# Kernel tuning notes

Measured on AMD Instinct MI355X. Metric: run time of the kernel, lower is better.

Reference implementation:

```python
import jax, jax.numpy as jnp
import numpy as np

T, C, H, W, CI = 4, 64, 96, 96, 16
PS, WS, STR0 = 7, 21, 4
KS, KA = 100, 100
SCALE = 10.0


def conv1x1(x, w, b):
    # x: [T,C,H,W], w: [O,C]
    return jnp.einsum('tchw,oc->tohw', x, w) + b[None, :, None, None]


def unfold_clip(x, ps):
    # clipped-boundary unfold: [T,C,H,W] -> [T, H*W, C*ps*ps]
    t, c, h, w = x.shape
    d = jnp.arange(ps)
    ii = jnp.clip(jnp.arange(h)[:, None] + d[None, :], 0, h - 1)  # [H,ps]
    jj = jnp.clip(jnp.arange(w)[:, None] + d[None, :], 0, w - 1)  # [W,ps]
    p = x[:, :, ii]            # [T,C,H,ps,W]
    p = p[:, :, :, :, jj]      # [T,C,H,ps,W,ps]
    p = jnp.transpose(p, (0, 2, 4, 1, 3, 5))  # [T,H,W,C,ps,ps]
    return p.reshape(t, h * w, c * ps * ps)


def setup_inputs() -> dict:
    key = jax.random.key(0)
    ks = jax.random.split(key, 9)
    s = lambda fan: 1.0 / np.sqrt(fan)
    return {
        'vid': jax.random.normal(ks[0], (T, C, H, W), jnp.float32),
        'g_w': jax.random.normal(ks[1], (CI, C), jnp.float32) * s(C),
        'g_b': jax.random.normal(ks[2], (CI,), jnp.float32) * 0.01,
        'theta_w': jax.random.normal(ks[3], (CI, C), jnp.float32) * s(C),
        'theta_b': jax.random.normal(ks[4], (CI,), jnp.float32) * 0.01,
        'phi_w': jax.random.normal(ks[5], (CI, C), jnp.float32) * s(C),
        'phi_b': jax.random.normal(ks[6], (CI,), jnp.float32) * 0.01,
        'W_w': jax.random.normal(ks[7], (C, CI), jnp.float32) * s(CI),
        'W_b': jax.random.normal(ks[8], (C,), jnp.float32) * 0.01,
    }


def reference(vid, g_w, g_b, theta_w, theta_b, phi_w, phi_b, W_w, W_b):
    t, c, h, w = vid.shape
    b1 = conv1x1(vid, g_w, g_b)          # query features  (g)
    b2 = conv1x1(vid, theta_w, theta_b)  # value features  (theta)
    b3 = conv1x1(vid, phi_w, phi_b)      # key features    (phi)

    b1u = unfold_clip(b1, PS)  # [T,HW,D]
    b2u = unfold_clip(b2, PS)
    b3u = unfold_clip(b3, PS)

    # query grid (stride0)
    qi, qj = jnp.meshgrid(jnp.arange(0, h, STR0), jnp.arange(0, w, STR0), indexing='ij')
    qi, qj = qi.reshape(-1), qj.reshape(-1)
    nq = qi.shape[0]
    qflat = qi * w + qj
    b1q = b1u[:, qflat]  # [T,nq,D]

    # centered spatial search window (stride1=1), clipped bounds
    off = jnp.arange(WS) - WS // 2
    ci = jnp.clip(qi[:, None] + off[None, :], 0, h - 1)  # [nq,WS]
    cj = jnp.clip(qj[:, None] + off[None, :], 0, w - 1)
    cand = (ci[:, :, None] * w + cj[:, None, :]).reshape(nq, WS * WS)

    # patch inner-product dists, one window offset at a time (memory-lean)
    def score(cidx):  # cidx: [nq]
        return jnp.einsum('tqd,tqd->tq', b1q, b3u[:, cidx])
    dists = jax.lax.map(score, cand.T)           # [WS*WS,T,nq]
    dists = jnp.transpose(dists, (1, 2, 0))      # [T,nq,WS*WS]

    vals, idx = jax.lax.top_k(dists, KS)
    vals, idx = vals[..., :KA], idx[..., :KA]
    yi = jax.nn.softmax(vals * SCALE, axis=-1)   # [T,nq,KA]

    pos = jnp.take_along_axis(jnp.broadcast_to(cand[None], (t,) + cand.shape), idx, axis=-1)
    patches = b2u[jnp.arange(t)[:, None, None], pos]   # [T,nq,KA,D]
    zi = jnp.einsum('tqk,tqkd->tqd', yi, patches)      # [T,nq,D]

    # fold: overlap-add scatter + counts normalization
    zi = zi.reshape(t, nq, CI, PS, PS).transpose(0, 2, 1, 3, 4).reshape(t, CI, nq * PS * PS)
    d = jnp.arange(PS)
    pi = jnp.clip(qi[:, None] + d[None, :], 0, h - 1)
    pj = jnp.clip(qj[:, None] + d[None, :], 0, w - 1)
    pix = (pi[:, :, None] * w + pj[:, None, :]).reshape(-1)
    acc = jnp.zeros((t, CI, h * w), vid.dtype).at[:, :, pix].add(zi)
    Z = jnp.zeros((h * w,), vid.dtype).at[pix].add(1.0)
    y = (acc / Z).reshape(t, CI, h, w)

    return vid + conv1x1(y, W_w, W_b)
```

## Files before the change

### kernel.cpp

```cpp
#include <hip/hip_runtime.h>
#include <hip/hip_bf16.h>
#include <hip/hip_fp16.h>
#include <math.h>

typedef __hip_bfloat16 bf16;
typedef unsigned int u32;
typedef unsigned long long u64;
typedef __attribute__((ext_vector_type(8))) short short8;
typedef __attribute__((ext_vector_type(4))) float float4v;

#define T_   4
#define C_   64
#define H_   96
#define W_   96
#define CI_  16
#define HW_  9216
#define NC_  441
#define K_   100
#define HSEL 0x07060302u
#define LSEL 0x05040100u

__device__ __forceinline__ float ldbf(const void* p, int i) { return __bfloat162float(((const bf16*)p)[i]); }
__device__ __forceinline__ float ldf (const void* p, int i) { return ((const float*)p)[i]; }

__device__ __forceinline__ unsigned short f2bf(float x) {
    union { float f; u32 u; } a; a.f = x;
    u32 r = a.u + 0x7FFF + ((a.u >> 16) & 1);
    return (unsigned short)(r >> 16);
}
__device__ __forceinline__ float bf2f(unsigned short s) {
    union { u32 u; float f; } a; a.u = ((u32)s) << 16;
    return a.f;
}
__device__ __forceinline__ u32 packbf(float x) {
    unsigned short h = f2bf(x);
    unsigned short l = f2bf(x - bf2f(h));
    return ((u32)h << 16) | (u32)l;
}
__device__ __forceinline__ u32 okey(float f) {
    u32 u = __float_as_uint(f);
    return u ^ ((u & 0x80000000u) ? 0xFFFFFFFFu : 0x80000000u);
}
__device__ __forceinline__ float unokey(u32 k) {
    u32 u = (k & 0x80000000u) ? (k ^ 0x80000000u) : ~k;
    return __uint_as_float(u);
}
__device__ __forceinline__ int cntdim(int x) {
    int c = 0;
#pragma unroll
    for (int pp = 0; pp < 7; pp++) {
        int q = x - pp;
        c += (q >= 0 && q <= 92 && ((q & 3) == 0)) ? 1 : 0;
    }
    if (x == 95) c += 3;
    return c;
}

__device__ __forceinline__ int detect_flag(const void* vid, int tid, int* sflag) {
    if (tid < 64) {
        unsigned short w = ((const unsigned short*)vid)[tid * 2];
        int e = (w >> 7) & 0xFF;
        int sane = ((e >= 100 && e <= 140) || ((w & 0x7FFF) == 0)) ? 1 : 0;
#pragma unroll
        for (int off = 1; off < 64; off <<= 1) sane += __shfl_xor(sane, off);
        if (tid == 0) *sflag = (sane >= 48) ? 1 : 0;
    }
    __syncthreads();
    return *sflag;
}

__global__ __launch_bounds__(256) void conv3_k(const void* vid, const void* gw, const void* gb,
                                               const void* tw, const void* tb, const void* pw,
                                               const void* pb,
                                               u32* __restrict__ B1p, __half* __restrict__ B2h,
                                               u32* __restrict__ B3p, float* __restrict__ ACCb)
{
    __shared__ __align__(16) float w[3120];
    __shared__ int sflag;
    int tid = threadIdx.x;
    int isbf = detect_flag(vid, tid, &sflag);
    for (int i = tid; i < 3120; i += 256) {
        float v;
        if (isbf) {
            if (i < 1024) v = ldbf(gw, i);
            else if (i < 2048) v = ldbf(tw, i - 1024);
            else if (i < 3072) v = ldbf(pw, i - 2048);
            else if (i < 3088) v = ldbf(gb, i - 3072);
            else if (i < 3104) v = ldbf(tb, i - 3088);
            else v = ldbf(pb, i - 3104);
        } else {
            if (i < 1024) v = ldf(gw, i);
            else if (i < 2048) v = ldf(tw, i - 1024);
            else if (i < 3072) v = ldf(pw, i - 2048);
            else if (i < 3088) v = ldf(gb, i - 3072);
            else if (i < 3104) v = ldf(tb, i - 3088);
            else v = ldf(pb, i - 3104);
        }
        int d;
        if (i < 3072) {
            int conv = i >> 10;
            int idx  = i & 1023;
            int o = idx >> 6, c = idx & 63;
            d = conv * 1024 + c * 16 + o;
        } else d = i;
        w[d] = v;
    }
    __syncthreads();

    {
        float4v z = {0.f, 0.f, 0.f, 0.f};
        *(float4v*)(ACCb + (blockIdx.x * 256 + tid) * 4) = z;
    }

    int lane = tid & 63, og = tid >> 6;
    int g0 = blockIdx.x * 64 + lane;
    int t = g0 / HW_, pix = g0 - t * HW_;

    float a1[4], a2[4], a3[4];
#pragma unroll
    for (int k = 0; k < 4; k++) {
        a1[k] = w[3072 + og * 4 + k];
        a2[k] = w[3088 + og * 4 + k];
        a3[k] = w[3104 + og * 4 + k];
    }
    int base = t * C_ * HW_ + pix;
#pragma unroll 16
    for (int c = 0; c < C_; c++) {
        float v = isbf ? ldbf(vid, base + c * HW_) : ldf(vid, base + c * HW_);
        float4v w1 = *(const float4v*)&w[c * 16 + og * 4];
        float4v w2 = *(const float4v*)&w[1024 + c * 16 + og * 4];
        float4v w3 = *(const float4v*)&w[2048 + c * 16 + og * 4];
#pragma unroll
        for (int k = 0; k < 4; k++) {
            a1[k] += v * w1[k];
            a2[k] += v * w2[k];
            a3[k] += v * w3[k];
        }
    }
    int ob = g0 * 16 + og * 4;
    uint4 p1, p3;
    p1.x = packbf(a1[0]); p1.y = packbf(a1[1]); p1.z = packbf(a1[2]); p1.w = packbf(a1[3]);
    p3.x = packbf(a3[0]); p3.y = packbf(a3[1]); p3.z = packbf(a3[2]); p3.w = packbf(a3[3]);
    *(uint4*)(B1p + ob) = p1;
    *(uint4*)(B3p + ob) = p3;
    __half2 h01 = __floats2half2_rn(a2[0], a2[1]);
    __half2 h23 = __floats2half2_rn(a2[2], a2[3]);
    uint2 p2;
    p2.x = *(u32*)&h01; p2.y = *(u32*)&h23;
    *(uint2*)(B2h + ob) = p2;
}

__global__ __launch_bounds__(512, 6) void attn_k(const u32* __restrict__ B1p,
                                                 const __half* __restrict__ B2h,
                                                 const u32* __restrict__ B3p,
                                                 float* __restrict__ ACCb)
{
    __shared__ __align__(16) char SM[51344];
    short*   Win  = (short*)SM;
    __half2* Wp   = (__half2*)SM;
    float*   Sc   = (float*)(SM + 32768);
    float*   Cb   = (float*)(SM + 39824);
    int*     hist = (int*)(SM + 39824);
    float*   yiw  = (float*)(SM + 48016);
    int*     pab  = (int*)(SM + 49616);
    int*     ctl  = (int*)(SM + 51216);

    int tid = threadIdx.x;
    int tile = blockIdx.x, t = blockIdx.y;
    int qy = tile / 12, qx = tile - qy * 12;
    int qi = qy * 8, qj = qx * 8;

    const u32*    B1t = B1p + t * HW_ * 16;
    const __half* B2t = B2h + t * HW_ * 16;
    const u32*    B3t = B3p + t * HW_ * 16;

    int lane = tid & 63, wv = tid >> 6;
    int nn = lane & 15, qsel = nn >> 3, pjn = nn & 7;
    int koff = (lane >> 4) * 8;

    for (int pos = tid; pos < 1024; pos += 512) {
        int row = pos >> 5, col = pos & 31;
        int vr = min(max(qi - 10 + row, 0), 95);
        int vc = min(max(qj - 10 + col, 0), 95);
        const u32* src = B3t + (vr * 96 + vc) * 16;
        uint4 U0 = *(const uint4*)src,       U1 = *(const uint4*)(src + 4);
        uint4 U2 = *(const uint4*)(src + 8), U3 = *(const uint4*)(src + 12);
        uint4 A, B;
        A.x = __builtin_amdgcn_perm(U0.y, U0.x, HSEL);
        A.y = __builtin_amdgcn_perm(U0.w, U0.z, HSEL);
        A.z = __builtin_amdgcn_perm(U1.y, U1.x, HSEL);
        A.w = __builtin_amdgcn_perm(U1.w, U1.z, HSEL);
        B.x = __builtin_amdgcn_perm(U2.y, U2.x, HSEL);
        B.y = __builtin_amdgcn_perm(U2.w, U2.z, HSEL);
        B.z = __builtin_amdgcn_perm(U3.y, U3.x, HSEL);
        B.w = __builtin_amdgcn_perm(U3.w, U3.z, HSEL);
        *(uint4*)(Win + pos * 16)     = A;
        *(uint4*)(Win + pos * 16 + 8) = B;
    }
    __syncthreads();

#pragma unroll 1
    for (int ri = 0; ri < 2; ri++) {
        short8 Bh[4], Bl[4];
        int qiq = qi + 4 * ri, qjq = qj + 4 * qsel;
#pragma unroll
        for (int s = 0; s < 4; s++) {
            int kk0 = s * 32 + koff;
            int pi = kk0 >> 4, c0 = kk0 & 15;
            uint4 U0 = {0, 0, 0, 0}, U1 = {0, 0, 0, 0};
            if (pjn < 7 && pi < 7) {
                const u32* src = B1t + (min(qiq + pi, 95) * 96 + min(qjq + pjn, 95)) * 16 + c0;
                U0 = *(const uint4*)src;
                U1 = *(const uint4*)(src + 4);
            }
            union { uint4 u; short8 s8; } hc, lc;
            hc.u.x = __builtin_amdgcn_perm(U0.y, U0.x, HSEL);
            hc.u.y = __builtin_amdgcn_perm(U0.w, U0.z, HSEL);
            hc.u.z = __builtin_amdgcn_perm(U1.y, U1.x, HSEL);
            hc.u.w = __builtin_amdgcn_perm(U1.w, U1.z, HSEL);
            lc.u.x = __builtin_amdgcn_perm(U0.y, U0.x, LSEL);
            lc.u.y = __builtin_amdgcn_perm(U0.w, U0.z, LSEL);
            lc.u.z = __builtin_amdgcn_perm(U1.y, U1.x, LSEL);
            lc.u.w = __builtin_amdgcn_perm(U1.w, U1.z, LSEL);
            Bh[s] = hc.s8; Bl[s] = lc.s8;
        }
        float* Cw = Cb + wv * 256;
        for (int r = wv; r < 21; r += 8) {
            float psum = 0.f;
            int v = (lane >= 21) ? 1 : 0;
            int b = lane - v * 21;
#pragma unroll
            for (int st = 0; st < 2; st++) {
                float4v acc = {0.f, 0.f, 0.f, 0.f};
#pragma unroll
                for (int s = 0; s < 4; s++) {
                    int arow = 4 * ri + r + 2 * s + (lane >> 5);
                    int aoff = (arow * 32 + st * 16 + nn) * 16 + ((lane >> 4) & 1) * 8;
                    short8 A = *(const short8*)(Win + aoff);
                    acc = __builtin_amdgcn_mfma_f32_16x16x32_bf16(A, Bh[s], acc, 0, 0, 0);
                    acc = __builtin_amdgcn_mfma_f32_16x16x32_bf16(A, Bl[s], acc, 0, 0, 0);
                }
                *(float4v*)(Cw + nn * 16 + (lane >> 4) * 4) = acc;
                if (lane < 42) {
#pragma unroll
                    for (int pj = 0; pj < 7; pj++) {
                        int sp = b + 4 * v + pj;
                        if ((sp >> 4) == st) psum += Cw[(8 * v + pj) * 16 + (sp & 15)];
                    }
                }
            }
            if (lane < 42) Sc[(ri * 2 + v) * 441 + r * 21 + b] = psum;
        }
    }
    __syncthreads();

    for (int pos = tid; pos < 1024; pos += 512) {
        int row = pos >> 5, col = pos & 31;
        int vr = min(max(qi - 10 + row, 0), 95);
        int vc = min(max(qj - 10 + col, 0), 95);
        const u32* src = B3t + (vr * 96 + vc) * 16;
        uint4 U0 = *(const uint4*)src,       U1 = *(const uint4*)(src + 4);
        uint4 U2 = *(const uint4*)(src + 8), U3 = *(const uint4*)(src + 12);
        uint4 A, B;
        A.x = __builtin_amdgcn_perm(U0.y, U0.x, LSEL);
        A.y = __builtin_amdgcn_perm(U0.w, U0.z, LSEL);
        A.z = __builtin_amdgcn_perm(U1.y, U1.x, LSEL);
        A.w = __builtin_amdgcn_perm(U1.w, U1.z, LSEL);
        B.x = __builtin_amdgcn_perm(U2.y, U2.x, LSEL);
        B.y = __builtin_amdgcn_perm(U2.w, U2.z, LSEL);
        B.z = __builtin_amdgcn_perm(U3.y, U3.x, LSEL);
        B.w = __builtin_amdgcn_perm(U3.w, U3.z, LSEL);
        *(uint4*)(Win + pos * 16)     = A;
        *(uint4*)(Win + pos * 16 + 8) = B;
    }
    __syncthreads();

#pragma unroll 1
    for (int ri = 0; ri < 2; ri++) {
        short8 Bh[4];
        int qiq = qi + 4 * ri, qjq = qj + 4 * qsel;
#pragma unroll
        for (int s = 0; s < 4; s++) {
            int kk0 = s * 32 + koff;
            int pi = kk0 >> 4, c0 = kk0 & 15;
            uint4 U0 = {0, 0, 0, 0}, U1 = {0, 0, 0, 0};
            if (pjn < 7 && pi < 7) {
                const u32* src = B1t + (min(qiq + pi, 95) * 96 + min(qjq + pjn, 95)) * 16 + c0;
                U0 = *(const uint4*)src;
                U1 = *(const uint4*)(src + 4);
            }
            union { uint4 u; short8 s8; } hc;
            hc.u.x = __builtin_amdgcn_perm(U0.y, U0.x, HSEL);
            hc.u.y = __builtin_amdgcn_perm(U0.w, U0.z, HSEL);
            hc.u.z = __builtin_amdgcn_perm(U1.y, U1.x, HSEL);
            hc.u.w = __builtin_amdgcn_perm(U1.w, U1.z, HSEL);
            Bh[s] = hc.s8;
        }
        float* Cw = Cb + wv * 256;
        for (int r = wv; r < 21; r += 8) {
            float psum = 0.f;
            int v = (lane >= 21) ? 1 : 0;
            int b = lane - v * 21;
#pragma unroll
            for (int st = 0; st < 2; st++) {
                float4v acc = {0.f, 0.f, 0.f, 0.f};
#pragma unroll
                for (int s = 0; s < 4; s++) {
                    int arow = 4 * ri + r + 2 * s + (lane >> 5);
                    int aoff = (arow * 32 + st * 16 + nn) * 16 + ((lane >> 4) & 1) * 8;
                    short8 A = *(const short8*)(Win + aoff);
                    acc = __builtin_amdgcn_mfma_f32_16x16x32_bf16(A, Bh[s], acc, 0, 0, 0);
                }
                *(float4v*)(Cw + nn * 16 + (lane >> 4) * 4) = acc;
                if (lane < 42) {
#pragma unroll
                    for (int pj = 0; pj < 7; pj++) {
                        int sp = b + 4 * v + pj;
                        if ((sp >> 4) == st) psum += Cw[(8 * v + pj) * 16 + (sp & 15)];
                    }
                }
            }
            if (lane < 42) Sc[(ri * 2 + v) * 441 + r * 21 + b] += psum;
        }
    }
    __syncthreads();

    int g = wv & 3;
    int ri2 = g >> 1, ci2 = g & 1;
    int qiq = qi + 4 * ri2, qjq = qj + 4 * ci2;
    int alo = max(0, 10 - qiq), ahi = min(20, 105 - qiq);
    int blo = max(0, 10 - qjq), bhi = min(20, 105 - qjq);
    u64 am0 = 0, am1 = 0;

    if (wv >= 4) {
        for (int pos = tid - 256; pos < 992; pos += 256) {
            int row = pos >> 5, col = pos & 31;
            int vr = min(max(qi - 10 + row, 0), 95);
            int vc = min(max(qj - 10 + col, 0), 95);
            const __half* src = B2t + (vr * 96 + vc) * 16;
            *(int4*)(Wp + pos * 8)     = *(const int4*)src;
            *(int4*)(Wp + pos * 8 + 4) = *(const int4*)(src + 8);
        }
    } else {
        u32 kreg[7]; int ni = 0;
        u32 kmax = 0;
        for (int i = lane; i < NC_; i += 64) {
            int aa = i / 21, bb = i - aa * 21;
            int ae = min(max(aa, alo), ahi), be = min(max(bb, blo), bhi);
            u32 k = okey(Sc[g * 441 + ae * 21 + be]);
            kmax = max(kmax, k);
            kreg[ni++] = k;
        }
#pragma unroll
        for (int off = 1; off < 64; off <<= 1) kmax = max(kmax, (u32)__shfl_xor((int)kmax, off));

        {
            int4 zz = {0, 0, 0, 0};
            *(int4*)(hist + g * 256 + lane * 4) = zz;
            if (lane < 8) ctl[g * 8 + lane] = (lane == 1) ? K_ : 0;
        }
        asm volatile("s_waitcnt lgkmcnt(0)" ::: "memory");

#pragma unroll 1
        for (int ps = 3; ps >= 2; ps--) {
            u32 pref  = (u32)ctl[g * 8];
            int need0 = ctl[g * 8 + 1];
            for (int a = 0; a < ni; a++) {
                u32 k = kreg[a];
                if (ps == 3 || (k >> ((ps + 1) * 8)) == pref)
                    atomicAdd(&hist[g * 256 + ((k >> (ps * 8)) & 255)], 1);
            }
            asm volatile("s_waitcnt lgkmcnt(0)" ::: "memory");
            int4 hv = *(int4*)(hist + g * 256 + lane * 4);
            int local = hv.x + hv.y + hv.z + hv.w;
            int s = local;
#pragma unroll
            for (int off = 1; off < 64; off <<= 1) {
                int tt = __shfl_down(s, off);
                if (lane + off < 64) s += tt;
            }
            int c4 = s - local;
            int c3 = c4 + hv.w, c2 = c3 + hv.z, c1 = c2 + hv.y, c0 = s;
            int cums[5] = {c0, c1, c2, c3, c4};
            int hk[4] = {hv.x, hv.y, hv.z, hv.w};
#pragma unroll
            for (int k = 0; k < 4; k++) {
                if (cums[k] >= need0 && cums[k + 1] < need0) {
                    int newneed = need0 - cums[k + 1];
                    ctl[g * 8]     = (int)((pref << 8) | (u32)(lane * 4 + k));
                    ctl[g * 8 + 1] = newneed;
                    if (newneed == hk[k] || ps == 2) { ctl[g * 8 + 3] = 1; ctl[g * 8 + 2] = 8 * ps; }
                }
            }
            int4 zz = {0, 0, 0, 0};
            *(int4*)(hist + g * 256 + lane * 4) = zz;
            asm volatile("s_waitcnt lgkmcnt(0)" ::: "memory");
            if (ctl[g * 8 + 3]) break;
        }

        {
            u32 theta = (u32)ctl[g * 8];
            int shift = ctl[g * 8 + 2];
            int need  = ctl[g * 8 + 1];
            int base  = K_ - need;
            int a2 = 0;
            for (int i = lane; i < NC_; i += 64) {
                u32 k = kreg[a2++];
                u32 hp = k >> shift;
                int slot = -1;
                if (hp > theta) slot = atomicAdd(&ctl[g * 8 + 4], 1);
                else if (hp == theta) {
                    int j = atomicAdd(&ctl[g * 8 + 5], 1);
                    if (j < need) slot = base + j;
                }
                if (slot >= 0) {
                    int a = i / 21, b = i - a * 21;
                    int ae = min(max(a, alo), ahi), be = min(max(b, blo), bhi);
                    yiw[g * 100 + slot] = unokey(k);
                    pab[g * 100 + slot] = ((ae + 4 * ri2) << 8) | (be + 4 * ci2);
                }
            }
            asm volatile("s_waitcnt lgkmcnt(0)" ::: "memory");
            float m = unokey(kmax);
            float wa  = expf((yiw[g * 100 + lane] - m) * 10.f);
            float wb2 = (lane < 36) ? expf((yiw[g * 100 + 64 + lane] - m) * 10.f) : 0.f;
            float ssum = wa + wb2;
#pragma unroll
            for (int off = 1; off < 64; off <<= 1) ssum += __shfl_xor(ssum, off);
            float inv = 1.f / ssum;
            float wan = wa * inv, wbn = wb2 * inv;
            yiw[g * 100 + lane] = wan;
            if (lane < 36) yiw[g * 100 + 64 + lane] = wbn;
            am0 = __ballot(wan != 0.f);
            am1 = __ballot((lane < 36) && (wbn != 0.f));
            asm volatile("s_waitcnt lgkmcnt(0)" ::: "memory");
        }
    }
    __syncthreads();
    if (wv >= 4) return;

    if (lane < 49) {
        int rsel = lane & 1;
        int pi2 = lane / 7, pj2 = lane - pi2 * 7;
        __half2 z[8];
#pragma unroll
        for (int j = 0; j < 8; j++) z[j] = __float2half2_rn(0.f);
#pragma unroll 1
        for (int half = 0; half < 2; half++) {
            u64 mm = half ? am1 : am0;
            int kb = half ? 64 : 0;
            while (mm) {
                int k = kb + (__ffsll(mm) - 1);
                mm &= mm - 1;
                float y = yiw[g * 100 + k];
                int pp = pab[g * 100 + k];
                int row = (pp >> 8) + pi2, col = (pp & 255) + pj2;
                const __half2* cell = Wp + (row * 32 + col) * 8;
                int4 A0 = *(const int4*)(cell + rsel * 4);
                int4 A1 = *(const int4*)(cell + 4 - rsel * 4);
                const __half2* pa  = (const __half2*)&A0;
                const __half2* pb2 = (const __half2*)&A1;
                __half2 yh = __float2half2_rn(y);
#pragma unroll
                for (int j = 0; j < 4; j++) {
                    z[j]     = __hfma2(pa[j],  yh, z[j]);
                    z[4 + j] = __hfma2(pb2[j], yh, z[4 + j]);
                }
            }
        }
        int orow = min(qiq + pi2, 95), ocol = min(qjq + pj2, 95);
        float* dst = ACCb + t * CI_ * HW_ + orow * 96 + ocol;
        int c0 = rsel * 8, c1 = 8 - c0;
#pragma unroll
        for (int jh = 0; jh < 4; jh++) {
            atomicAdd(dst + (c0 + 2 * jh) * HW_,     __low2float(z[jh]));
            atomicAdd(dst + (c0 + 2 * jh + 1) * HW_, __high2float(z[jh]));
            atomicAdd(dst + (c1 + 2 * jh) * HW_,     __low2float(z[4 + jh]));
            atomicAdd(dst + (c1 + 2 * jh + 1) * HW_, __high2float(z[4 + jh]));
        }
    }
}

__global__ __launch_bounds__(256) void out_k(const void* vid, const void* Ww, const void* Wb,
                                             const float* __restrict__ ACCb, void* out)
{
    __shared__ float w[1088];
    __shared__ int sflag;
    int tid = threadIdx.x;
    int isbf = detect_flag(vid, tid, &sflag);
    if (isbf) { for (int i = tid; i < 1088; i += 256) w[i] = (i < 1024) ? ldbf(Ww, i) : ldbf(Wb, i - 1024); }
    else      { for (int i = tid; i < 1088; i += 256) w[i] = (i < 1024) ? ldf (Ww, i) : ldf (Wb, i - 1024); }
    __syncthreads();

    int lane5 = tid & 31, oct = tid >> 5;
    int g0 = blockIdx.x * 32 + lane5;
    int t = g0 / HW_, pix = g0 - t * HW_;
    int pi = pix / 96, pj = pix - pi * 96;
    float invz = 1.f / (float)(cntdim(pi) * cntdim(pj));

    float y[CI_];
    int ab = t * CI_ * HW_ + pix;
#pragma unroll
    for (int ci = 0; ci < CI_; ci++) y[ci] = ACCb[ab + ci * HW_] * invz;

    int vb = t * C_ * HW_ + pix;
#pragma unroll
    for (int co = oct * 8; co < oct * 8 + 8; co++) {
        float s = w[1024 + co];
#pragma unroll
        for (int ci = 0; ci < CI_; ci++) s += w[co * 16 + ci] * y[ci];
        int idx = vb + co * HW_;
        float vv = isbf ? ldbf(vid, idx) : ldf(vid, idx);
        float r = vv + s;
        if (isbf) ((bf16*)out)[idx] = __float2bfloat16(r);
        else      ((float*)out)[idx] = r;
    }
}

extern "C" void kernel_launch(void* const* d_in, const int* in_sizes, int n_in,
                              void* d_out, int out_size, void* d_ws, size_t ws_size,
                              hipStream_t stream)
{
    char* ws = (char*)d_ws;
    u32*    B1p  = (u32*)ws;
    __half* B2h  = (__half*)(ws + 2359296);
    u32*    B3p  = (u32*)(ws + 3538944);
    float*  ACCb = (float*)(ws + 5898240);

    conv3_k<<<dim3(576), dim3(256), 0, stream>>>(d_in[0], d_in[1], d_in[2], d_in[3], d_in[4],
                                                 d_in[5], d_in[6], B1p, B2h, B3p, ACCb);
    attn_k<<<dim3(144, T_), dim3(512), 0, stream>>>(B1p, B2h, B3p, ACCb);
    out_k<<<dim3(1152), dim3(256), 0, stream>>>(d_in[0], d_in[7], d_in[8], ACCb, d_out);
}
```

Measured before the change: 164.9 us.

## Halve attention tile height to double block count and shrink LDS

Each attention block now covers a 4x8 query region (2 queries) instead of 8x8 (4 queries), so the grid doubles to 288x4 blocks. The key window staged in LDS shrinks from 32 to 28 rows, LDS drops to about 40KB and the launch-bounds occupancy hint rises to 8. The aim is more blocks in flight and better latency hiding. In exchange, the overlap in the search window is reused across fewer queries, so more global reloads and redundant window staging occur, and only 2 waves do the aggregation instead of 4.

```diff
diff --git a/kernel.cpp b/kernel.cpp
--- a/kernel.cpp
+++ b/kernel.cpp
@@ -150,25 +150,25 @@
     *(uint2*)(B2h + ob) = p2;
 }
 
-__global__ __launch_bounds__(512, 6) void attn_k(const u32* __restrict__ B1p,
+__global__ __launch_bounds__(512, 8) void attn_k(const u32* __restrict__ B1p,
                                                  const __half* __restrict__ B2h,
                                                  const u32* __restrict__ B3p,
                                                  float* __restrict__ ACCb)
 {
-    __shared__ __align__(16) char SM[51344];
+    __shared__ __align__(16) char SM[40400];
     short*   Win  = (short*)SM;
     __half2* Wp   = (__half2*)SM;
-    float*   Sc   = (float*)(SM + 32768);
-    float*   Cb   = (float*)(SM + 39824);
-    int*     hist = (int*)(SM + 39824);
-    float*   yiw  = (float*)(SM + 48016);
-    int*     pab  = (int*)(SM + 49616);
-    int*     ctl  = (int*)(SM + 51216);
+    float*   Sc   = (float*)(SM + 28672);
+    float*   Cb   = (float*)(SM + 32208);
+    int*     hist = (int*)(SM + 32208);
+    float*   yiw  = (float*)(SM + 34256);
+    int*     pab  = (int*)(SM + 35056);
+    int*     ctl  = (int*)(SM + 35856);
 
     int tid = threadIdx.x;
     int tile = blockIdx.x, t = blockIdx.y;
     int qy = tile / 12, qx = tile - qy * 12;
-    int qi = qy * 8, qj = qx * 8;
+    int qi = qy * 4, qj = qx * 8;
 
     const u32*    B1t = B1p + t * HW_ * 16;
     const __half* B2t = B2h + t * HW_ * 16;
@@ -178,7 +178,7 @@
     int nn = lane & 15, qsel = nn >> 3, pjn = nn & 7;
     int koff = (lane >> 4) * 8;
 
-    for (int pos = tid; pos < 1024; pos += 512) {
+    for (int pos = tid; pos < 896; pos += 512) {
         int row = pos >> 5, col = pos & 31;
         int vr = min(max(qi - 10 + row, 0), 95);
         int vc = min(max(qj - 10 + col, 0), 95);
@@ -199,17 +199,16 @@
     }
     __syncthreads();
 
-#pragma unroll 1
-    for (int ri = 0; ri < 2; ri++) {
+    {
         short8 Bh[4], Bl[4];
-        int qiq = qi + 4 * ri, qjq = qj + 4 * qsel;
+        int qjq = qj + 4 * qsel;
 #pragma unroll
         for (int s = 0; s < 4; s++) {
             int kk0 = s * 32 + koff;
             int pi = kk0 >> 4, c0 = kk0 & 15;
             uint4 U0 = {0, 0, 0, 0}, U1 = {0, 0, 0, 0};
             if (pjn < 7 && pi < 7) {
-                const u32* src = B1t + (min(qiq + pi, 95) * 96 + min(qjq + pjn, 95)) * 16 + c0;
+                const u32* src = B1t + (min(qi + pi, 95) * 96 + min(qjq + pjn, 95)) * 16 + c0;
                 U0 = *(const uint4*)src;
                 U1 = *(const uint4*)(src + 4);
             }
@@ -234,7 +233,7 @@
                 float4v acc = {0.f, 0.f, 0.f, 0.f};
 #pragma unroll
                 for (int s = 0; s < 4; s++) {
-                    int arow = 4 * ri + r + 2 * s + (lane >> 5);
+                    int arow = r + 2 * s + (lane >> 5);
                     int aoff = (arow * 32 + st * 16 + nn) * 16 + ((lane >> 4) & 1) * 8;
                     short8 A = *(const short8*)(Win + aoff);
                     acc = __builtin_amdgcn_mfma_f32_16x16x32_bf16(A, Bh[s], acc, 0, 0, 0);
@@ -249,12 +248,12 @@
                     }
                 }
             }
-            if (lane < 42) Sc[(ri * 2 + v) * 441 + r * 21 + b] = psum;
-        }
-    }
-    __syncthreads();
-
-    for (int pos = tid; pos < 1024; pos += 512) {
+            if (lane < 42) Sc[v * 441 + r * 21 + b] = psum;
+        }
+    }
+    __syncthreads();
+
+    for (int pos = tid; pos < 896; pos += 512) {
         int row = pos >> 5, col = pos & 31;
         int vr = min(max(qi - 10 + row, 0), 95);
         int vc = min(max(qj - 10 + col, 0), 95);
@@ -275,17 +274,16 @@
     }
     __syncthreads();
 
-#pragma unroll 1
-    for (int ri = 0; ri < 2; ri++) {
+    {
         short8 Bh[4];
-        int qiq = qi + 4 * ri, qjq = qj + 4 * qsel;
+        int qjq = qj + 4 * qsel;
 #pragma unroll
         for (int s = 0; s < 4; s++) {
             int kk0 = s * 32 + koff;
             int pi = kk0 >> 4, c0 = kk0 & 15;
             uint4 U0 = {0, 0, 0, 0}, U1 = {0, 0, 0, 0};
             if (pjn < 7 && pi < 7) {
-                const u32* src = B1t + (min(qiq + pi, 95) * 96 + min(qjq + pjn, 95)) * 16 + c0;
+                const u32* src = B1t + (min(qi + pi, 95) * 96 + min(qjq + pjn, 95)) * 16 + c0;
                 U0 = *(const uint4*)src;
                 U1 = *(const uint4*)(src + 4);
             }
@@ -306,7 +304,7 @@
                 float4v acc = {0.f, 0.f, 0.f, 0.f};
 #pragma unroll
                 for (int s = 0; s < 4; s++) {
-                    int arow = 4 * ri + r + 2 * s + (lane >> 5);
+                    int arow = r + 2 * s + (lane >> 5);
                     int aoff = (arow * 32 + st * 16 + nn) * 16 + ((lane >> 4) & 1) * 8;
                     short8 A = *(const short8*)(Win + aoff);
                     acc = __builtin_amdgcn_mfma_f32_16x16x32_bf16(A, Bh[s], acc, 0, 0, 0);
@@ -320,20 +318,19 @@
                     }
                 }
             }
-            if (lane < 42) Sc[(ri * 2 + v) * 441 + r * 21 + b] += psum;
-        }
-    }
-    __syncthreads();
-
-    int g = wv & 3;
-    int ri2 = g >> 1, ci2 = g & 1;
-    int qiq = qi + 4 * ri2, qjq = qj + 4 * ci2;
-    int alo = max(0, 10 - qiq), ahi = min(20, 105 - qiq);
-    int blo = max(0, 10 - qjq), bhi = min(20, 105 - qjq);
+            if (lane < 42) Sc[v * 441 + r * 21 + b] += psum;
+        }
+    }
+    __syncthreads();
+
+    int g = wv;
+    int qjq2 = qj + 4 * (wv & 1);
+    int alo = max(0, 10 - qi), ahi = min(20, 105 - qi);
+    int blo = max(0, 10 - qjq2), bhi = min(20, 105 - qjq2);
     u64 am0 = 0, am1 = 0;
 
-    if (wv >= 4) {
-        for (int pos = tid - 256; pos < 992; pos += 256) {
+    if (wv >= 2) {
+        for (int pos = tid - 128; pos < 864; pos += 384) {
             int row = pos >> 5, col = pos & 31;
             int vr = min(max(qi - 10 + row, 0), 95);
             int vc = min(max(qj - 10 + col, 0), 95);
@@ -417,7 +414,7 @@
                     int a = i / 21, b = i - a * 21;
                     int ae = min(max(a, alo), ahi), be = min(max(b, blo), bhi);
                     yiw[g * 100 + slot] = unokey(k);
-                    pab[g * 100 + slot] = ((ae + 4 * ri2) << 8) | (be + 4 * ci2);
+                    pab[g * 100 + slot] = (ae << 8) | (be + 4 * g);
                 }
             }
             asm volatile("s_waitcnt lgkmcnt(0)" ::: "memory");
@@ -437,7 +434,7 @@
         }
     }
     __syncthreads();
-    if (wv >= 4) return;
+    if (wv >= 2) return;
 
     if (lane < 49) {
         int rsel = lane & 1;
@@ -468,7 +465,7 @@
                 }
             }
         }
-        int orow = min(qiq + pi2, 95), ocol = min(qjq + pj2, 95);
+        int orow = min(qi + pi2, 95), ocol = min(qjq2 + pj2, 95);
         float* dst = ACCb + t * CI_ * HW_ + orow * 96 + ocol;
         int c0 = rsel * 8, c1 = 8 - c0;
 #pragma unroll
@@ -529,6 +526,6 @@
 
     conv3_k<<<dim3(576), dim3(256), 0, stream>>>(d_in[0], d_in[1], d_in[2], d_in[3], d_in[4],
                                                  d_in[5], d_in[6], B1p, B2h, B3p, ACCb);
-    attn_k<<<dim3(144, T_), dim3(512), 0, stream>>>(B1p, B2h, B3p, ACCb);
+    attn_k<<<dim3(288, T_), dim3(512), 0, stream>>>(B1p, B2h, B3p, ACCb);
     out_k<<<dim3(1152), dim3(256), 0, stream>>>(d_in[0], d_in[7], d_in[8], ACCb, d_out);
 }
```

Measured after the change: 178.4 us. +8.1%, slower.
